# Kernel tuning notes

Measured on AMD Instinct MI355X. Metric: run time of the kernel, lower is better.

## Reference

```python
import jax, jax.numpy as jnp
import numpy as np

DIM = 1024

def setup_inputs() -> dict:
    key = jax.random.key(0)
    ks = jax.random.split(key, 8)
    B, Sx, Sy, D = 4, 2048, 2048, DIM
    s = 1.0 / np.sqrt(D)
    return {
        "x": jax.random.normal(ks[0], (B, Sx, D), jnp.float32),
        "y": jax.random.normal(ks[1], (B, Sy, D), jnp.float32),
        "Wq": jax.random.normal(ks[2], (D, D), jnp.float32) * s,
        "bq": jnp.zeros((D,), jnp.float32),
        "Wk": jax.random.normal(ks[3], (D, D), jnp.float32) * s,
        "bk": jnp.zeros((D,), jnp.float32),
        "Wv": jax.random.normal(ks[4], (D, D), jnp.float32) * s,
        "bv": jnp.zeros((D,), jnp.float32),
    }

def reference(x, y, Wq, bq, Wk, bk, Wv, bv):
    D = x.shape[-1]
    scale = jnp.sqrt(jnp.asarray(D, x.dtype))
    Q = jnp.einsum('bsd,de->bse', x, Wq) + bq  # [B,Sx,D]
    K = jnp.einsum('btd,de->bte', y, Wk) + bk  # [B,Sy,D]
    V = jnp.einsum('btd,de->bte', y, Wv) + bv  # [B,Sy,D]
    scores = jnp.einsum('bse,bte->bst', Q, K) / scale  # [B,Sx,Sy]
    probs = jax.nn.softmax(scores, axis=-1)
    out = jnp.einsum('bst,bte->bse', probs, V)  # [B,Sx,D]
    return out
```

## Files before the change

kernel.cpp:

```cpp
#include <hip/hip_runtime.h>

typedef __bf16 bf16x8_t __attribute__((ext_vector_type(8)));
typedef float f32x4_t __attribute__((ext_vector_type(4)));
typedef unsigned short ushort_t;

__device__ __forceinline__ unsigned short f2bf(float f) {
  unsigned u = __float_as_uint(f);
  u = (u + 0x7FFFu + ((u >> 16) & 1u)) >> 16;
  return (unsigned short)u;
}
__device__ __forceinline__ float bf2f(unsigned short h) {
  return __uint_as_float(((unsigned)h) << 16);
}

__device__ __forceinline__ void gload16(const void* g, void* l) {
  __builtin_amdgcn_global_load_lds(
      (const __attribute__((address_space(1))) unsigned int*)g,
      (__attribute__((address_space(3))) unsigned int*)l, 16, 0, 0);
}

#define BARRIER() __builtin_amdgcn_s_barrier()
#define LGKM0()                                        \
  do {                                                 \
    asm volatile("s_waitcnt lgkmcnt(0)" ::: "memory"); \
    __builtin_amdgcn_sched_barrier(0);                 \
  } while (0)

template<bool OUT_BF16, bool HAS_BIAS>
__global__ __launch_bounds__(512, 2)
void gemm256(const ushort_t* __restrict__ A, const ushort_t* __restrict__ Bt,
             void* __restrict__ Cp, const float* __restrict__ bias,
             int gx, int gy, int K, int lda, int ldb, int ldc,
             long sA, long sB, long sC, float alpha)
{
  __shared__ __align__(16) ushort_t sm[2 * 32768];
  const int tid = threadIdx.x;
  const int lane = tid & 63;
  const int w = tid >> 6;
  const int wr = w >> 2, wc = w & 3;

  const int per = gridDim.x >> 3;
  int wg = blockIdx.x;
  wg = (wg & 7) * per + (wg >> 3);
  const int bz = wg / (gx * gy);
  const int rr = wg - bz * gx * gy;
  const int by = rr / gx, bx = rr - by * gx;
  const int bm = by * 256, bn = bx * 256;

  const int srr = lane >> 3;
  const int csw = ((lane & 7) ^ srr) << 3;
  const ushort_t* pA = A + (long)bz * sA + (long)(bm + w * 16 + srr) * lda + csw;
  const ushort_t* pB = Bt + (long)bz * sB + (long)(bn + w * 16 + srr) * ldb + csw;

  auto stA = [&](int buf, int h, int t) {
    const ushort_t* g = pA + (long)(h * 128) * lda + t * 64;
    ushort_t* d = sm + buf * 32768 + h * 8192 + w * 1024;
    gload16(g, d);
    gload16(g + 8 * lda, d + 512);
  };
  auto stB = [&](int buf, int h, int t) {
    const ushort_t* g = pB + (long)(h * 128) * ldb + t * 64;
    ushort_t* d = sm + buf * 32768 + 16384 + h * 8192 + w * 1024;
    gload16(g, d);
    gload16(g + 8 * ldb, d + 512);
  };

  const int q = lane >> 4, x7 = lane & 7;
  const int cx0 = ((0 + q) ^ x7) << 3;
  const int cx1 = ((4 + q) ^ x7) << 3;
  const int abase = wr * 8192 + (lane & 15) * 64;
  const int bbase = 16384 + wc * 4096 + (lane & 15) * 64;

  f32x4_t acc[8][4];
  const f32x4_t z4 = {0.f, 0.f, 0.f, 0.f};
#pragma unroll
  for (int m = 0; m < 8; ++m)
#pragma unroll
    for (int n = 0; n < 4; ++n) acc[m][n] = z4;

  bf16x8_t a[8], blo[4], bhi[4];

  stA(0, 0, 0); stA(0, 1, 0); stB(0, 0, 0); stB(0, 1, 0);
  stB(1, 0, 1); stB(1, 1, 1); stA(1, 0, 1);
  asm volatile("s_waitcnt vmcnt(6)" ::: "memory");
  __builtin_amdgcn_sched_barrier(0);
  BARRIER();

#define LDX(off) __builtin_bit_cast(bf16x8_t, *(const uint4*)(s + (off)))

  const int nt = K >> 6;
  for (int t = 0; t < nt; ++t) {
    const int buf = t & 1;
    const ushort_t* s = sm + buf * 32768;

#pragma unroll
    for (int mf = 0; mf < 4; ++mf) {
      a[mf * 2]     = LDX(abase + mf * 1024 + cx0);
      a[mf * 2 + 1] = LDX(abase + mf * 1024 + cx1);
    }
#pragma unroll
    for (int nf = 0; nf < 2; ++nf) {
      blo[nf * 2]     = LDX(bbase + nf * 1024 + cx0);
      blo[nf * 2 + 1] = LDX(bbase + nf * 1024 + cx1);
    }
    if (t + 1 < nt) stA(buf ^ 1, 1, t + 1);
    BARRIER();
    LGKM0();
    __builtin_amdgcn_s_setprio(1);
#pragma unroll
    for (int mf = 0; mf < 4; ++mf)
#pragma unroll
      for (int nf = 0; nf < 2; ++nf) {
        acc[mf][nf] = __builtin_amdgcn_mfma_f32_16x16x32_bf16(a[mf * 2], blo[nf * 2], acc[mf][nf], 0, 0, 0);
        acc[mf][nf] = __builtin_amdgcn_mfma_f32_16x16x32_bf16(a[mf * 2 + 1], blo[nf * 2 + 1], acc[mf][nf], 0, 0, 0);
      }
    __builtin_amdgcn_s_setprio(0);
    BARRIER();

#pragma unroll
    for (int nf = 0; nf < 2; ++nf) {
      bhi[nf * 2]     = LDX(bbase + (nf + 2) * 1024 + cx0);
      bhi[nf * 2 + 1] = LDX(bbase + (nf + 2) * 1024 + cx1);
    }
    if (t + 2 < nt) stB(buf, 0, t + 2);
    BARRIER();
    LGKM0();
    __builtin_amdgcn_s_setprio(1);
#pragma unroll
    for (int mf = 0; mf < 4; ++mf)
#pragma unroll
      for (int nf = 0; nf < 2; ++nf) {
        acc[mf][nf + 2] = __builtin_amdgcn_mfma_f32_16x16x32_bf16(a[mf * 2], bhi[nf * 2], acc[mf][nf + 2], 0, 0, 0);
        acc[mf][nf + 2] = __builtin_amdgcn_mfma_f32_16x16x32_bf16(a[mf * 2 + 1], bhi[nf * 2 + 1], acc[mf][nf + 2], 0, 0, 0);
      }
    __builtin_amdgcn_s_setprio(0);
    BARRIER();

#pragma unroll
    for (int mf = 0; mf < 4; ++mf) {
      a[mf * 2]     = LDX(abase + (mf + 4) * 1024 + cx0);
      a[mf * 2 + 1] = LDX(abase + (mf + 4) * 1024 + cx1);
    }
    if (t + 2 < nt) stB(buf, 1, t + 2);
    BARRIER();
    LGKM0();
    __builtin_amdgcn_s_setprio(1);
#pragma unroll
    for (int mf = 0; mf < 4; ++mf)
#pragma unroll
      for (int nf = 0; nf < 2; ++nf) {
        acc[mf + 4][nf + 2] = __builtin_amdgcn_mfma_f32_16x16x32_bf16(a[mf * 2], bhi[nf * 2], acc[mf + 4][nf + 2], 0, 0, 0);
        acc[mf + 4][nf + 2] = __builtin_amdgcn_mfma_f32_16x16x32_bf16(a[mf * 2 + 1], bhi[nf * 2 + 1], acc[mf + 4][nf + 2], 0, 0, 0);
      }
    __builtin_amdgcn_s_setprio(0);
    BARRIER();

    if (t + 2 < nt) stA(buf, 0, t + 2);
    __builtin_amdgcn_s_setprio(1);
#pragma unroll
    for (int mf = 0; mf < 4; ++mf)
#pragma unroll
      for (int nf = 0; nf < 2; ++nf) {
        acc[mf + 4][nf] = __builtin_amdgcn_mfma_f32_16x16x32_bf16(a[mf * 2], blo[nf * 2], acc[mf + 4][nf], 0, 0, 0);
        acc[mf + 4][nf] = __builtin_amdgcn_mfma_f32_16x16x32_bf16(a[mf * 2 + 1], blo[nf * 2 + 1], acc[mf + 4][nf], 0, 0, 0);
      }
    __builtin_amdgcn_s_setprio(0);
    if (t + 1 < nt) {
      if (t + 2 < nt) asm volatile("s_waitcnt vmcnt(6)" ::: "memory");
      else            asm volatile("s_waitcnt vmcnt(0)" ::: "memory");
      __builtin_amdgcn_sched_barrier(0);
    }
    BARRIER();
  }
#undef LDX

  const long zC = (long)bz * sC;
  const int r0 = q * 4;
  const int c0 = lane & 15;
#pragma unroll
  for (int mf = 0; mf < 8; ++mf) {
    const int grow0 = bm + wr * 128 + mf * 16 + r0;
#pragma unroll
    for (int nf = 0; nf < 4; ++nf) {
      const int gcol = bn + wc * 64 + nf * 16 + c0;
      float bv_ = 0.f;
      if constexpr (HAS_BIAS) bv_ = bias[gcol];
#pragma unroll
      for (int i = 0; i < 4; ++i) {
        const float v = acc[mf][nf][i] * alpha + bv_;
        if constexpr (OUT_BF16) {
          ((ushort_t*)Cp)[zC + (long)(grow0 + i) * ldc + gcol] = f2bf(v);
        } else {
          ((float*)Cp)[zC + (long)(grow0 + i) * ldc + gcol] = v;
        }
      }
    }
  }
}

template<bool OUT_BF16, bool HAS_BIAS>
__global__ __launch_bounds__(256, 3)
void gemm_nt(const ushort_t* __restrict__ A, const ushort_t* __restrict__ Bt,
             void* __restrict__ Cp, const float* __restrict__ bias,
             int gx, int gy, int K, int lda, int ldb, int ldc,
             long sA, long sB, long sC, float alpha)
{
  __shared__ __align__(16) ushort_t smem[2][8192];
  const int tid = threadIdx.x;
  const int lane = tid & 63;
  const int wave = tid >> 6;

  const int per = gridDim.x >> 3;
  int wg = blockIdx.x;
  wg = (wg & 7) * per + (wg >> 3);
  const int bz = wg / (gx * gy);
  const int rr = wg - bz * gx * gy;
  const int by = rr / gx, bx = rr - by * gx;
  const int bm = by * 128, bn = bx * 128;

  const ushort_t* Ab = A + (long)bz * sA;
  const ushort_t* Bb = Bt + (long)bz * sB;

  const int r_s0 = wave * 16 + (lane >> 2);
  const int r_s1 = (wave + 4) * 16 + (lane >> 2);
  const int c_s0 = (((lane & 3) ^ ((r_s0 >> 1) & 3)) << 3);
  const int c_s1 = (((lane & 3) ^ ((r_s1 >> 1) & 3)) << 3);
  const ushort_t* gA0 = Ab + (long)(bm + r_s0) * lda + c_s0;
  const ushort_t* gA1 = Ab + (long)(bm + r_s1) * lda + c_s1;
  const ushort_t* gB0 = Bb + (long)(bn + r_s0) * ldb + c_s0;
  const ushort_t* gB1 = Bb + (long)(bn + r_s1) * ldb + c_s1;

  auto stage = [&](int kt, int buf) {
    const int k0 = kt << 5;
    ushort_t* s = smem[buf];
    gload16(gA0 + k0, s + wave * 512);
    gload16(gA1 + k0, s + (wave + 4) * 512);
    gload16(gB0 + k0, s + 4096 + wave * 512);
    gload16(gB1 + k0, s + 4096 + (wave + 4) * 512);
  };

  const int wr = wave >> 1, wc = wave & 1;
  int offA[4], offB[4];
#pragma unroll
  for (int m = 0; m < 4; ++m) {
    const int row = wr * 64 + m * 16 + (lane & 15);
    offA[m] = row * 32 + ((((lane >> 4) ^ ((row >> 1) & 3))) << 3);
  }
#pragma unroll
  for (int n = 0; n < 4; ++n) {
    const int row = wc * 64 + n * 16 + (lane & 15);
    offB[n] = 4096 + row * 32 + ((((lane >> 4) ^ ((row >> 1) & 3))) << 3);
  }

  f32x4_t acc[4][4];
  const f32x4_t z4 = {0.f, 0.f, 0.f, 0.f};
#pragma unroll
  for (int m = 0; m < 4; ++m)
#pragma unroll
    for (int n = 0; n < 4; ++n) acc[m][n] = z4;

  stage(0, 0);
  __syncthreads();

  const int nt = K >> 5;
  for (int kt = 0; kt < nt; ++kt) {
    const int cur = kt & 1;
    if (kt + 1 < nt) stage(kt + 1, cur ^ 1);
    const ushort_t* s = smem[cur];
    bf16x8_t af[4], bfv[4];
#pragma unroll
    for (int m = 0; m < 4; ++m)
      af[m] = __builtin_bit_cast(bf16x8_t, *(const uint4*)(s + offA[m]));
#pragma unroll
    for (int n = 0; n < 4; ++n)
      bfv[n] = __builtin_bit_cast(bf16x8_t, *(const uint4*)(s + offB[n]));
#pragma unroll
    for (int m = 0; m < 4; ++m)
#pragma unroll
      for (int n = 0; n < 4; ++n)
        acc[m][n] = __builtin_amdgcn_mfma_f32_16x16x32_bf16(af[m], bfv[n], acc[m][n], 0, 0, 0);
    __syncthreads();
  }

  const long zC = (long)bz * sC;
  const int r0 = (lane >> 4) * 4;
  const int c0 = lane & 15;
#pragma unroll
  for (int m = 0; m < 4; ++m) {
    const int grow0 = bm + wr * 64 + m * 16 + r0;
#pragma unroll
    for (int n = 0; n < 4; ++n) {
      const int gcol = bn + wc * 64 + n * 16 + c0;
      float bv_ = 0.f;
      if constexpr (HAS_BIAS) bv_ = bias[gcol];
#pragma unroll
      for (int i = 0; i < 4; ++i) {
        const float v = acc[m][n][i] * alpha + bv_;
        if constexpr (OUT_BF16) {
          ((ushort_t*)Cp)[zC + (long)(grow0 + i) * ldc + gcol] = f2bf(v);
        } else {
          ((float*)Cp)[zC + (long)(grow0 + i) * ldc + gcol] = v;
        }
      }
    }
  }
}

__global__ __launch_bounds__(256)
void conv_f32_bf16(const float* __restrict__ in, ushort_t* __restrict__ out) {
  const long i = (long)blockIdx.x * 256 + threadIdx.x;
  const float4 a = ((const float4*)in)[i * 2];
  const float4 b = ((const float4*)in)[i * 2 + 1];
  uint4 o;
  o.x = (unsigned)f2bf(a.x) | ((unsigned)f2bf(a.y) << 16);
  o.y = (unsigned)f2bf(a.z) | ((unsigned)f2bf(a.w) << 16);
  o.z = (unsigned)f2bf(b.x) | ((unsigned)f2bf(b.y) << 16);
  o.w = (unsigned)f2bf(b.z) | ((unsigned)f2bf(b.w) << 16);
  ((uint4*)out)[i] = o;
}

__global__ __launch_bounds__(256)
void wtrans(const float* __restrict__ W, ushort_t* __restrict__ Wt) {
  __shared__ float tile[32][33];
  const int bx = blockIdx.x * 32;
  const int by = blockIdx.y * 32;
  const int t = threadIdx.x;
  const int c = t & 31, r0 = t >> 5;
#pragma unroll
  for (int i = 0; i < 4; ++i)
    tile[r0 + i * 8][c] = W[(long)(by + r0 + i * 8) * 1024 + bx + c];
  __syncthreads();
#pragma unroll
  for (int i = 0; i < 4; ++i)
    Wt[(long)(bx + r0 + i * 8) * 1024 + by + c] = f2bf(tile[c][r0 + i * 8]);
}

__global__ __launch_bounds__(256)
void bconcat(const float* __restrict__ a, const float* __restrict__ b,
             float* __restrict__ o) {
  const int i = blockIdx.x * 256 + threadIdx.x;
  o[i] = (i < 1024) ? a[i] : b[i - 1024];
}

__global__ __launch_bounds__(256)
void transpose_bf16(const ushort_t* __restrict__ in, ushort_t* __restrict__ out,
                    int ld_in, int ld_out, long in_bs, long out_bs) {
  __shared__ ushort_t tt[64][65];
  in += (long)blockIdx.z * in_bs;
  out += (long)blockIdx.z * out_bs;
  const int r0 = blockIdx.y * 64, c0 = blockIdx.x * 64;
  const int tc = threadIdx.x & 31;
  const int tr = threadIdx.x >> 5;
#pragma unroll
  for (int i = 0; i < 8; ++i) {
    const unsigned v = *(const unsigned*)(in + (long)(r0 + tr + 8 * i) * ld_in + c0 + tc * 2);
    tt[tr + 8 * i][tc * 2] = (ushort_t)(v & 0xffff);
    tt[tr + 8 * i][tc * 2 + 1] = (ushort_t)(v >> 16);
  }
  __syncthreads();
#pragma unroll
  for (int i = 0; i < 8; ++i) {
    const unsigned v = (unsigned)tt[tc * 2][tr + 8 * i] |
                       ((unsigned)tt[tc * 2 + 1][tr + 8 * i] << 16);
    *(unsigned*)(out + (long)(c0 + tr + 8 * i) * ld_out + r0 + tc * 2) = v;
  }
}

__global__ __launch_bounds__(256)
void softmax_rows(ushort_t* __restrict__ S) {
  const long row = blockIdx.x;
  ushort_t* p = S + row * 2048;
  const int t = threadIdx.x;
  uint4 v = ((uint4*)p)[t];
  ushort_t* hp = (ushort_t*)&v;
  float f[8];
#pragma unroll
  for (int j = 0; j < 8; ++j) f[j] = bf2f(hp[j]);

  float m = f[0];
#pragma unroll
  for (int j = 1; j < 8; ++j) m = fmaxf(m, f[j]);
#pragma unroll
  for (int s = 32; s; s >>= 1) m = fmaxf(m, __shfl_xor(m, s, 64));
  __shared__ float redm[4];
  __shared__ float reds[4];
  const int wave = t >> 6, lane = t & 63;
  if (lane == 0) redm[wave] = m;
  __syncthreads();
  m = fmaxf(fmaxf(redm[0], redm[1]), fmaxf(redm[2], redm[3]));

  float sum = 0.f;
#pragma unroll
  for (int j = 0; j < 8; ++j) { f[j] = __expf(f[j] - m); sum += f[j]; }
#pragma unroll
  for (int s = 32; s; s >>= 1) sum += __shfl_xor(sum, s, 64);
  if (lane == 0) reds[wave] = sum;
  __syncthreads();
  sum = reds[0] + reds[1] + reds[2] + reds[3];
  const float inv = 1.0f / sum;
#pragma unroll
  for (int j = 0; j < 8; ++j) hp[j] = f2bf(f[j] * inv);
  ((uint4*)p)[t] = v;
}

extern "C" void kernel_launch(void* const* d_in, const int* in_sizes, int n_in,
                              void* d_out, int out_size, void* d_ws, size_t ws_size,
                              hipStream_t stream) {
  const float* x  = (const float*)d_in[0];
  const float* y  = (const float*)d_in[1];
  const float* Wq = (const float*)d_in[2];
  const float* bq = (const float*)d_in[3];
  const float* Wk = (const float*)d_in[4];
  const float* bk = (const float*)d_in[5];
  const float* Wv = (const float*)d_in[6];
  const float* bv = (const float*)d_in[7];
  float* out = (float*)d_out;

  const int D = 1024;
  const long MB_ = 1l << 20;

  ushort_t* ws  = (ushort_t*)d_ws;
  ushort_t* Wqt = ws;
  ushort_t* Wkv = ws + 1 * MB_;
  ushort_t* Wvt = ws + 2 * MB_;
  ushort_t* Qb  = ws + 3 * MB_;
  ushort_t* KV  = ws + 11 * MB_;
  ushort_t* yb  = ws + 27 * MB_;
  ushort_t* Vt  = ws + 27 * MB_;
  ushort_t* xb  = ws + 35 * MB_;
  ushort_t* Sb  = ws + 35 * MB_;
  float*    bkv = (float*)(ws + 51 * MB_);

  dim3 blk(256);

  conv_f32_bf16<<<dim3(4096), blk, 0, stream>>>(x, xb);
  conv_f32_bf16<<<dim3(4096), blk, 0, stream>>>(y, yb);
  wtrans<<<dim3(32, 32), blk, 0, stream>>>(Wq, Wqt);
  wtrans<<<dim3(32, 32), blk, 0, stream>>>(Wk, Wkv);
  wtrans<<<dim3(32, 32), blk, 0, stream>>>(Wv, Wvt);
  bconcat<<<dim3(8), blk, 0, stream>>>(bk, bv, bkv);

  gemm256<true, true><<<dim3(128), dim3(512), 0, stream>>>(
      xb, Wqt, Qb, bq, 4, 32, D, D, D, D, 0, 0, 0, 1.0f);
  gemm256<true, true><<<dim3(256), dim3(512), 0, stream>>>(
      yb, Wkv, KV, bkv, 8, 32, D, D, D, 2048, 0, 0, 0, 1.0f);
  transpose_bf16<<<dim3(16, 32, 4), blk, 0, stream>>>(
      KV + 1024, Vt, 2048, 2048, 2048l * 2048, 1024l * 2048);

  gemm256<true, false><<<dim3(256), dim3(512), 0, stream>>>(
      Qb, KV, Sb, nullptr, 8, 8, D, D, 2048, 2048,
      2048l * 1024, 2048l * 2048, 2048l * 2048, 0.03125f);

  softmax_rows<<<dim3(8192), blk, 0, stream>>>(Sb);

  gemm_nt<false, false><<<dim3(512), blk, 0, stream>>>(
      Sb, Vt, out, nullptr, 8, 16, 2048, 2048, 2048, D,
      2048l * 2048, 1024l * 2048, 2048l * 1024, 1.0f);
}
```

Baseline: 203.5 us.

## Replace 128x128 NT GEMM with 8-wave 128x256 staged-pipeline kernel; merge prep launches

Replaces the 4-wave 128x128 gemm_nt with an 8-wave gemm_hs that computes 128x256 tiles using BK=64. It splits each k-step into four MFMA phases interleaved with LDS fragment loads, staggers the global-to-LDS prefetch of A and B, and raises wave priority around the MFMA blocks. The new kernel now runs both the Q projection and the probs·V GEMM. The intent is better data reuse and overlap of memory with MFMA work. Separately, the two fp32-to-bf16 conversions are merged into one launch, as are the three weight transposes, to cut launch overhead. In exchange, each block uses more LDS and fewer blocks launch (256 per GEMM), which lowers occupancy.

```diff
diff --git a/kernel.cpp b/kernel.cpp
--- a/kernel.cpp
+++ b/kernel.cpp
@@ -199,16 +199,17 @@
 }
 
 template<bool OUT_BF16, bool HAS_BIAS>
-__global__ __launch_bounds__(256, 3)
-void gemm_nt(const ushort_t* __restrict__ A, const ushort_t* __restrict__ Bt,
+__global__ __launch_bounds__(512, 2)
+void gemm_hs(const ushort_t* __restrict__ A, const ushort_t* __restrict__ Bt,
              void* __restrict__ Cp, const float* __restrict__ bias,
              int gx, int gy, int K, int lda, int ldb, int ldc,
              long sA, long sB, long sC, float alpha)
 {
-  __shared__ __align__(16) ushort_t smem[2][8192];
+  __shared__ __align__(16) ushort_t sm[2 * 24576];
   const int tid = threadIdx.x;
   const int lane = tid & 63;
-  const int wave = tid >> 6;
+  const int w = tid >> 6;
+  const int wr = w >> 2, wc = w & 3;
 
   const int per = gridDim.x >> 3;
   int wg = blockIdx.x;
@@ -216,41 +217,33 @@
   const int bz = wg / (gx * gy);
   const int rr = wg - bz * gx * gy;
   const int by = rr / gx, bx = rr - by * gx;
-  const int bm = by * 128, bn = bx * 128;
-
-  const ushort_t* Ab = A + (long)bz * sA;
-  const ushort_t* Bb = Bt + (long)bz * sB;
-
-  const int r_s0 = wave * 16 + (lane >> 2);
-  const int r_s1 = (wave + 4) * 16 + (lane >> 2);
-  const int c_s0 = (((lane & 3) ^ ((r_s0 >> 1) & 3)) << 3);
-  const int c_s1 = (((lane & 3) ^ ((r_s1 >> 1) & 3)) << 3);
-  const ushort_t* gA0 = Ab + (long)(bm + r_s0) * lda + c_s0;
-  const ushort_t* gA1 = Ab + (long)(bm + r_s1) * lda + c_s1;
-  const ushort_t* gB0 = Bb + (long)(bn + r_s0) * ldb + c_s0;
-  const ushort_t* gB1 = Bb + (long)(bn + r_s1) * ldb + c_s1;
-
-  auto stage = [&](int kt, int buf) {
-    const int k0 = kt << 5;
-    ushort_t* s = smem[buf];
-    gload16(gA0 + k0, s + wave * 512);
-    gload16(gA1 + k0, s + (wave + 4) * 512);
-    gload16(gB0 + k0, s + 4096 + wave * 512);
-    gload16(gB1 + k0, s + 4096 + (wave + 4) * 512);
+  const int bm = by * 128, bn = bx * 256;
+
+  const int srr = lane >> 3;
+  const int csw = ((lane & 7) ^ srr) << 3;
+  const ushort_t* pA = A + (long)bz * sA + (long)(bm + w * 16 + srr) * lda + csw;
+  const ushort_t* pB = Bt + (long)bz * sB + (long)(bn + w * 32 + srr) * ldb + csw;
+
+  auto stA = [&](int buf, int t) {
+    const ushort_t* g = pA + t * 64;
+    ushort_t* d = sm + buf * 24576 + w * 1024;
+    gload16(g, d);
+    gload16(g + 8 * lda, d + 512);
   };
-
-  const int wr = wave >> 1, wc = wave & 1;
-  int offA[4], offB[4];
-#pragma unroll
-  for (int m = 0; m < 4; ++m) {
-    const int row = wr * 64 + m * 16 + (lane & 15);
-    offA[m] = row * 32 + ((((lane >> 4) ^ ((row >> 1) & 3))) << 3);
-  }
-#pragma unroll
-  for (int n = 0; n < 4; ++n) {
-    const int row = wc * 64 + n * 16 + (lane & 15);
-    offB[n] = 4096 + row * 32 + ((((lane >> 4) ^ ((row >> 1) & 3))) << 3);
-  }
+  auto stB = [&](int buf, int t) {
+    const ushort_t* g = pB + t * 64;
+    ushort_t* d = sm + buf * 24576 + 8192 + w * 2048;
+    gload16(g, d);
+    gload16(g + 8 * ldb, d + 512);
+    gload16(g + 16 * ldb, d + 1024);
+    gload16(g + 24 * ldb, d + 1536);
+  };
+
+  const int q = lane >> 4, x7 = lane & 7;
+  const int cx0 = ((0 + q) ^ x7) << 3;
+  const int cx1 = ((4 + q) ^ x7) << 3;
+  const int abase = wr * 4096 + (lane & 15) * 64;
+  const int bbase = 8192 + wc * 4096 + (lane & 15) * 64;
 
   f32x4_t acc[4][4];
   const f32x4_t z4 = {0.f, 0.f, 0.f, 0.f};
@@ -259,43 +252,101 @@
 #pragma unroll
     for (int n = 0; n < 4; ++n) acc[m][n] = z4;
 
-  stage(0, 0);
-  __syncthreads();
-
-  const int nt = K >> 5;
-  for (int kt = 0; kt < nt; ++kt) {
-    const int cur = kt & 1;
-    if (kt + 1 < nt) stage(kt + 1, cur ^ 1);
-    const ushort_t* s = smem[cur];
-    bf16x8_t af[4], bfv[4];
-#pragma unroll
-    for (int m = 0; m < 4; ++m)
-      af[m] = __builtin_bit_cast(bf16x8_t, *(const uint4*)(s + offA[m]));
-#pragma unroll
-    for (int n = 0; n < 4; ++n)
-      bfv[n] = __builtin_bit_cast(bf16x8_t, *(const uint4*)(s + offB[n]));
-#pragma unroll
-    for (int m = 0; m < 4; ++m)
-#pragma unroll
-      for (int n = 0; n < 4; ++n)
-        acc[m][n] = __builtin_amdgcn_mfma_f32_16x16x32_bf16(af[m], bfv[n], acc[m][n], 0, 0, 0);
-    __syncthreads();
+  bf16x8_t a01[4], a23[4], blo[4], bhi[4];
+
+  stA(0, 0); stB(0, 0); stA(1, 1);
+  asm volatile("s_waitcnt vmcnt(2)" ::: "memory");
+  __builtin_amdgcn_sched_barrier(0);
+  BARRIER();
+
+#define LDX(off) __builtin_bit_cast(bf16x8_t, *(const uint4*)(s + (off)))
+
+  const int nt = K >> 6;
+  for (int t = 0; t < nt; ++t) {
+    const int buf = t & 1;
+    const ushort_t* s = sm + buf * 24576;
+
+    a01[0] = LDX(abase + cx0);        a01[1] = LDX(abase + cx1);
+    a01[2] = LDX(abase + 1024 + cx0); a01[3] = LDX(abase + 1024 + cx1);
+    blo[0] = LDX(bbase + cx0);        blo[1] = LDX(bbase + cx1);
+    blo[2] = LDX(bbase + 1024 + cx0); blo[3] = LDX(bbase + 1024 + cx1);
+    if (t + 1 < nt) stB(buf ^ 1, t + 1);
+    BARRIER();
+    LGKM0();
+    __builtin_amdgcn_s_setprio(1);
+#pragma unroll
+    for (int mf = 0; mf < 2; ++mf)
+#pragma unroll
+      for (int nf = 0; nf < 2; ++nf) {
+        acc[mf][nf] = __builtin_amdgcn_mfma_f32_16x16x32_bf16(a01[mf * 2], blo[nf * 2], acc[mf][nf], 0, 0, 0);
+        acc[mf][nf] = __builtin_amdgcn_mfma_f32_16x16x32_bf16(a01[mf * 2 + 1], blo[nf * 2 + 1], acc[mf][nf], 0, 0, 0);
+      }
+    __builtin_amdgcn_s_setprio(0);
+    BARRIER();
+
+    bhi[0] = LDX(bbase + 2048 + cx0); bhi[1] = LDX(bbase + 2048 + cx1);
+    bhi[2] = LDX(bbase + 3072 + cx0); bhi[3] = LDX(bbase + 3072 + cx1);
+    BARRIER();
+    LGKM0();
+    __builtin_amdgcn_s_setprio(1);
+#pragma unroll
+    for (int mf = 0; mf < 2; ++mf)
+#pragma unroll
+      for (int nf = 0; nf < 2; ++nf) {
+        acc[mf][nf + 2] = __builtin_amdgcn_mfma_f32_16x16x32_bf16(a01[mf * 2], bhi[nf * 2], acc[mf][nf + 2], 0, 0, 0);
+        acc[mf][nf + 2] = __builtin_amdgcn_mfma_f32_16x16x32_bf16(a01[mf * 2 + 1], bhi[nf * 2 + 1], acc[mf][nf + 2], 0, 0, 0);
+      }
+    __builtin_amdgcn_s_setprio(0);
+    BARRIER();
+
+    a23[0] = LDX(abase + 2048 + cx0); a23[1] = LDX(abase + 2048 + cx1);
+    a23[2] = LDX(abase + 3072 + cx0); a23[3] = LDX(abase + 3072 + cx1);
+    BARRIER();
+    LGKM0();
+    __builtin_amdgcn_s_setprio(1);
+#pragma unroll
+    for (int mf = 0; mf < 2; ++mf)
+#pragma unroll
+      for (int nf = 0; nf < 2; ++nf) {
+        acc[mf + 2][nf + 2] = __builtin_amdgcn_mfma_f32_16x16x32_bf16(a23[mf * 2], bhi[nf * 2], acc[mf + 2][nf + 2], 0, 0, 0);
+        acc[mf + 2][nf + 2] = __builtin_amdgcn_mfma_f32_16x16x32_bf16(a23[mf * 2 + 1], bhi[nf * 2 + 1], acc[mf + 2][nf + 2], 0, 0, 0);
+      }
+    __builtin_amdgcn_s_setprio(0);
+    BARRIER();
+
+    if (t + 2 < nt) stA(buf, t + 2);
+    __builtin_amdgcn_s_setprio(1);
+#pragma unroll
+    for (int mf = 0; mf < 2; ++mf)
+#pragma unroll
+      for (int nf = 0; nf < 2; ++nf) {
+        acc[mf + 2][nf] = __builtin_amdgcn_mfma_f32_16x16x32_bf16(a23[mf * 2], blo[nf * 2], acc[mf + 2][nf], 0, 0, 0);
+        acc[mf + 2][nf] = __builtin_amdgcn_mfma_f32_16x16x32_bf16(a23[mf * 2 + 1], blo[nf * 2 + 1], acc[mf + 2][nf], 0, 0, 0);
+      }
+    __builtin_amdgcn_s_setprio(0);
+    if (t + 1 < nt) {
+      if (t + 2 < nt) asm volatile("s_waitcnt vmcnt(2)" ::: "memory");
+      else            asm volatile("s_waitcnt vmcnt(0)" ::: "memory");
+      __builtin_amdgcn_sched_barrier(0);
+    }
+    BARRIER();
   }
+#undef LDX
 
   const long zC = (long)bz * sC;
-  const int r0 = (lane >> 4) * 4;
+  const int r0 = q * 4;
   const int c0 = lane & 15;
 #pragma unroll
-  for (int m = 0; m < 4; ++m) {
-    const int grow0 = bm + wr * 64 + m * 16 + r0;
-#pragma unroll
-    for (int n = 0; n < 4; ++n) {
-      const int gcol = bn + wc * 64 + n * 16 + c0;
+  for (int mf = 0; mf < 4; ++mf) {
+    const int grow0 = bm + wr * 64 + mf * 16 + r0;
+#pragma unroll
+    for (int nf = 0; nf < 4; ++nf) {
+      const int gcol = bn + wc * 64 + nf * 16 + c0;
       float bv_ = 0.f;
       if constexpr (HAS_BIAS) bv_ = bias[gcol];
 #pragma unroll
       for (int i = 0; i < 4; ++i) {
-        const float v = acc[m][n][i] * alpha + bv_;
+        const float v = acc[mf][nf][i] * alpha + bv_;
         if constexpr (OUT_BF16) {
           ((ushort_t*)Cp)[zC + (long)(grow0 + i) * ldc + gcol] = f2bf(v);
         } else {
@@ -307,20 +358,28 @@
 }
 
 __global__ __launch_bounds__(256)
-void conv_f32_bf16(const float* __restrict__ in, ushort_t* __restrict__ out) {
-  const long i = (long)blockIdx.x * 256 + threadIdx.x;
+void conv2(const float* __restrict__ x, const float* __restrict__ y,
+           ushort_t* __restrict__ xb, ushort_t* __restrict__ yb) {
+  const int b = blockIdx.x;
+  const float* in = (b < 4096) ? x : y;
+  ushort_t* out = (b < 4096) ? xb : yb;
+  const long i = (long)(b & 4095) * 256 + threadIdx.x;
   const float4 a = ((const float4*)in)[i * 2];
-  const float4 b = ((const float4*)in)[i * 2 + 1];
+  const float4 c = ((const float4*)in)[i * 2 + 1];
   uint4 o;
   o.x = (unsigned)f2bf(a.x) | ((unsigned)f2bf(a.y) << 16);
   o.y = (unsigned)f2bf(a.z) | ((unsigned)f2bf(a.w) << 16);
-  o.z = (unsigned)f2bf(b.x) | ((unsigned)f2bf(b.y) << 16);
-  o.w = (unsigned)f2bf(b.z) | ((unsigned)f2bf(b.w) << 16);
+  o.z = (unsigned)f2bf(c.x) | ((unsigned)f2bf(c.y) << 16);
+  o.w = (unsigned)f2bf(c.z) | ((unsigned)f2bf(c.w) << 16);
   ((uint4*)out)[i] = o;
 }
 
 __global__ __launch_bounds__(256)
-void wtrans(const float* __restrict__ W, ushort_t* __restrict__ Wt) {
+void wtrans3(const float* __restrict__ W0, const float* __restrict__ W1,
+             const float* __restrict__ W2, ushort_t* __restrict__ T0,
+             ushort_t* __restrict__ T1, ushort_t* __restrict__ T2) {
+  const float* W = (blockIdx.z == 0) ? W0 : (blockIdx.z == 1) ? W1 : W2;
+  ushort_t* Wt = (blockIdx.z == 0) ? T0 : (blockIdx.z == 1) ? T1 : T2;
   __shared__ float tile[32][33];
   const int bx = blockIdx.x * 32;
   const int by = blockIdx.y * 32;
@@ -433,15 +492,12 @@
 
   dim3 blk(256);
 
-  conv_f32_bf16<<<dim3(4096), blk, 0, stream>>>(x, xb);
-  conv_f32_bf16<<<dim3(4096), blk, 0, stream>>>(y, yb);
-  wtrans<<<dim3(32, 32), blk, 0, stream>>>(Wq, Wqt);
-  wtrans<<<dim3(32, 32), blk, 0, stream>>>(Wk, Wkv);
-  wtrans<<<dim3(32, 32), blk, 0, stream>>>(Wv, Wvt);
+  conv2<<<dim3(8192), blk, 0, stream>>>(x, y, xb, yb);
+  wtrans3<<<dim3(32, 32, 3), blk, 0, stream>>>(Wq, Wk, Wv, Wqt, Wkv, Wvt);
   bconcat<<<dim3(8), blk, 0, stream>>>(bk, bv, bkv);
 
-  gemm256<true, true><<<dim3(128), dim3(512), 0, stream>>>(
-      xb, Wqt, Qb, bq, 4, 32, D, D, D, D, 0, 0, 0, 1.0f);
+  gemm_hs<true, true><<<dim3(256), dim3(512), 0, stream>>>(
+      xb, Wqt, Qb, bq, 4, 64, D, D, D, D, 0, 0, 0, 1.0f);
   gemm256<true, true><<<dim3(256), dim3(512), 0, stream>>>(
       yb, Wkv, KV, bkv, 8, 32, D, D, D, 2048, 0, 0, 0, 1.0f);
   transpose_bf16<<<dim3(16, 32, 4), blk, 0, stream>>>(
@@ -453,7 +509,7 @@
 
   softmax_rows<<<dim3(8192), blk, 0, stream>>>(Sb);
 
-  gemm_nt<false, false><<<dim3(512), blk, 0, stream>>>(
-      Sb, Vt, out, nullptr, 8, 16, 2048, 2048, 2048, D,
+  gemm_hs<false, false><<<dim3(256), dim3(512), 0, stream>>>(
+      Sb, Vt, out, nullptr, 4, 16, 2048, 2048, 2048, D,
       2048l * 2048, 1024l * 2048, 2048l * 1024, 1.0f);
 }
```

After: 189.8 us. 1.07x faster.
